# Kernel tuning notes

Measured on AMD Instinct MI355X. Metric: run time of the kernel, lower is better.

Reference implementation:

```python
import jax, jax.numpy as jnp
import numpy as np

# B images, N objects/image, R relations/image; D=obj/rel feature dim, H=GGNN hidden,
# NO=num object classes, NR=num relation classes, T=GGNN time steps.
B, N, R, D, H, NO, NR, T = 8, 64, 2048, 4096, 512, 151, 51, 3


def setup_inputs() -> dict:
    key = jax.random.key(0)
    ks = jax.random.split(key, 24)
    nrm = lambda k, shp: jax.random.normal(k, shp, dtype=jnp.float32) * 0.02
    im_inds = jnp.repeat(jnp.arange(B, dtype=jnp.int32), N)          # sorted per-object image ids
    img_r = jnp.repeat(jnp.arange(B, dtype=jnp.int32), R)            # per-relation image ids
    pair = jax.random.randint(ks[0], (B * R, 2), 0, N, dtype=jnp.int32) + (img_r * N)[:, None]
    rel_inds = jnp.concatenate([img_r[:, None], pair], axis=1)        # [B*R, 3]
    return dict(
        im_inds=im_inds, rel_inds=rel_inds,
        obj_fmaps=jax.random.normal(ks[1], (B * N, D), jnp.float32),
        obj_logits=jax.random.normal(ks[2], (B * N, NO), jnp.float32),
        vr=jax.random.normal(ks[3], (B * R, D), jnp.float32),
        W_obj=nrm(ks[4], (D, H)), b_obj=jnp.zeros((H,), jnp.float32),
        W_rel=nrm(ks[5], (D, H)), b_rel=jnp.zeros((H,), jnp.float32),
        W_prob=nrm(ks[6], (NO, H)), b_prob=jnp.zeros((H,), jnp.float32),
        W_so=nrm(ks[7], (H, H)), W_oo=nrm(ks[8], (H, H)),
        W_rs=nrm(ks[9], (H, H)), W_ro=nrm(ks[10], (H, H)),
        Wz=nrm(ks[11], (H, H)), Uz=nrm(ks[12], (H, H)), bz=jnp.zeros((H,), jnp.float32),
        Wr=nrm(ks[13], (H, H)), Ur=nrm(ks[14], (H, H)), br=jnp.zeros((H,), jnp.float32),
        Wh=nrm(ks[15], (H, H)), Uh=nrm(ks[16], (H, H)), bh=jnp.zeros((H,), jnp.float32),
        W_out_rel=nrm(ks[17], (2 * H, H)), b_out_rel=jnp.zeros((H,), jnp.float32),
        W_cls_rel=nrm(ks[18], (H, NR)), b_cls_rel=jnp.zeros((NR,), jnp.float32),
        W_out_obj=nrm(ks[19], (2 * H, H)), b_out_obj=jnp.zeros((H,), jnp.float32),
        W_cls_obj=nrm(ks[20], (H, NO)), b_cls_obj=jnp.zeros((NO,), jnp.float32),
    )


def reference(im_inds, rel_inds, obj_fmaps, obj_logits, vr,
              W_obj, b_obj, W_rel, b_rel, W_prob, b_prob,
              W_so, W_oo, W_rs, W_ro,
              Wz, Uz, bz, Wr, Ur, br, Wh, Uh, bh,
              W_out_rel, b_out_rel, W_cls_rel, b_cls_rel,
              W_out_obj, b_out_obj, W_cls_obj, b_cls_obj):
    # obj_probs = softmax(obj_logits); project features + class distribution into GGNN hidden
    obj_probs = jax.nn.softmax(obj_logits, axis=-1)
    xo = (obj_fmaps @ W_obj + b_obj + obj_probs @ W_prob + b_prob).reshape(B, N, H)
    xr = (vr @ W_rel + b_rel).reshape(B, R, H)
    # per-image local indices: rel_inds[rel_s:rel_e, 1:] - obj_s
    off = (jnp.arange(B, dtype=rel_inds.dtype) * N)[:, None]
    subj = rel_inds[:, 1].reshape(B, R) - off
    objn = rel_inds[:, 2].reshape(B, R) - off

    def gru(h, m):
        z = jax.nn.sigmoid(m @ Wz + h @ Uz + bz)
        r = jax.nn.sigmoid(m @ Wr + h @ Ur + br)
        hh = jnp.tanh(m @ Wh + (r * h) @ Uh + bh)
        return (1.0 - z) * h + z * hh

    def per_image(xo_i, xr_i, s, o):
        ho, hr = xo_i, xr_i
        for _ in range(T):  # fixed recurrence depth (time_step_num)
            mr = ho[s] @ W_so + ho[o] @ W_oo                               # gather obj -> rel
            mo = (jax.ops.segment_sum(hr @ W_rs, s, num_segments=N)
                  + jax.ops.segment_sum(hr @ W_ro, o, num_segments=N))     # scatter rel -> obj
            ho, hr = gru(ho, mo), gru(hr, mr)
        rel_logits = jnp.tanh(jnp.concatenate([hr, xr_i], -1) @ W_out_rel + b_out_rel) @ W_cls_rel + b_cls_rel
        obj_ref = jnp.tanh(jnp.concatenate([ho, xo_i], -1) @ W_out_obj + b_out_obj) @ W_cls_obj + b_cls_obj
        return rel_logits, obj_ref

    rel_logits, obj_ref = jax.vmap(per_image)(xo, xr, subj, objn)
    rel_logits = rel_logits.reshape(B * R, NR)
    obj_ref = obj_ref.reshape(B * N, NO)
    scpred_softmax = jax.nn.softmax(rel_logits, axis=-1)
    scent_softmax = jax.nn.softmax(obj_ref, axis=-1)
    # sgcls, inference, no obj_labels: obj_preds = argmax over classes 1..NO-1, + 1
    obj_preds = jnp.argmax(obj_ref[:, 1:], axis=-1) + 1
    return (obj_ref, obj_preds, rel_logits, scpred_softmax, scent_softmax)
```

## Files before the change

### kernel.cpp

```cpp
#include <hip/hip_runtime.h>
#include <math.h>

#define Bn   8
#define Nn   64
#define Rn   2048
#define Dn   4096
#define Hn   512
#define NOc  151
#define NRc  51
#define Tt   3
#define BNt  (Bn*Nn)
#define BRt  (Bn*Rn)
#define Mall (BRt+BNt)

typedef __attribute__((ext_vector_type(8))) short short8;
typedef __attribute__((ext_vector_type(4))) float f32x4;

__device__ __forceinline__ float sigmf(float x){ return 1.0f/(1.0f+expf(-x)); }

__device__ __forceinline__ ushort f2bf_rne(float x){
  unsigned u = __float_as_uint(x);
  unsigned r = u + 0x7FFFu + ((u>>16)&1u);
  return (ushort)(r>>16);
}
__device__ __forceinline__ float bf2f(ushort h){
  return __uint_as_float(((unsigned)h)<<16);
}

__device__ __forceinline__ void async_ld16(const ushort* g, ushort* l){
  __builtin_amdgcn_global_load_lds(
      (const __attribute__((address_space(1))) unsigned int*)g,
      (__attribute__((address_space(3))) unsigned int*)l, 16, 0, 0);
}

template<int BM,int BN,int ASPLIT>
__global__ __launch_bounds__(256)
void gemm_b3(const float* __restrict__ Af,
             const ushort* __restrict__ Aph, const ushort* __restrict__ Apl,
             const ushort* __restrict__ Bhg, const ushort* __restrict__ Blg,
             float* __restrict__ Cf, const float* __restrict__ Cin,
             int M,int N,int K,int lda,int ldb,int ldc,
             const float* __restrict__ bias, const float* __restrict__ bias2,
             int act,int dupoff,
             ushort* __restrict__ Cph, ushort* __restrict__ Cpl,int ldcp,int dupp,
             int swz,int mode,const int* __restrict__ rel,
             const float* __restrict__ Gso,const float* __restrict__ G1,
             int brt,float* __restrict__ Zb,
             ushort* __restrict__ RHh,ushort* __restrict__ RHl,
             float* __restrict__ Hf,
             ushort* __restrict__ HXph,ushort* __restrict__ HXpl)
{
  constexpr int MT = BM/32, NT = BN/32;
  constexpr int NSEG = BN/16;
  constexpr int SEGW = NSEG/2;
  __shared__ ushort As[2][2][BM*32];
  __shared__ ushort Bs[2][2][BN*32];

  int bxi = blockIdx.x, byi = blockIdx.y;
  if (swz){
    int id  = byi*gridDim.x + bxi;
    int mch = gridDim.y >> 3;
    int xcd = id & 7, j = id >> 3;
    byi = xcd*mch + j % mch;
    bxi = j / mch;
  }
  const int tid  = threadIdx.x;
  const int lane = tid & 63;
  const int wid  = tid >> 6;
  const int quad = lane >> 4, l15 = lane & 15;
  const int wm = (wid>>1)*(BM/2), wn = (wid&1)*(BN/2);
  const int bm = byi*BM, bn = bxi*BN;

  constexpr int TPR = 256/BM, CPT = 32/TPR;
  const int ar = tid / TPR;
  const int ak = (tid % TPR) * CPT;
  const int grA = bm + ar;
  const int aswz = (ar>>1)&3;

  const ushort* bptr[SEGW];
#pragma unroll
  for (int i=0;i<SEGW;i++){
    int seg = i*4 + wid;
    int plane = (seg >= NSEG) ? 1 : 0;
    int ss = seg & (NSEG-1);
    int row = ss*16 + (lane>>2);
    int cg = (lane&3) ^ ((row>>1)&3);
    bptr[i] = (plane ? Blg : Bhg) + (size_t)(bn + row)*ldb + cg*8;
  }

  f32x4 acc[MT][NT];
#pragma unroll
  for (int i=0;i<MT;i++)
#pragma unroll
    for (int j=0;j<NT;j++) acc[i][j] = (f32x4){0.f,0.f,0.f,0.f};

  float  avf[ASPLIT ? 1 : CPT];
  short8 avh[ASPLIT ? CPT/8 : 1], avl[ASPLIT ? CPT/8 : 1];

  auto load_A = [&](int k0){
    if constexpr (ASPLIT){
      if (grA < M){
#pragma unroll
        for (int i=0;i<CPT/8;i++){
          avh[i] = *(const short8*)(Aph + (size_t)grA*lda + k0 + ak + i*8);
          avl[i] = *(const short8*)(Apl + (size_t)grA*lda + k0 + ak + i*8);
        }
      } else {
#pragma unroll
        for (int i=0;i<CPT/8;i++){
#pragma unroll
          for (int q=0;q<8;q++){ avh[i][q]=0; avl[i][q]=0; }
        }
      }
    } else {
      if (grA < M && ((lda&3)==0) && k0 + ak + CPT <= K) {
        const float* p = Af + (size_t)grA*lda + k0 + ak;
#pragma unroll
        for (int i=0;i<CPT/4;i++) ((float4*)avf)[i] = ((const float4*)p)[i];
      } else {
#pragma unroll
        for (int i=0;i<CPT;i++){
          int gk = k0+ak+i;
          avf[i] = (grA<M && gk<K) ? Af[(size_t)grA*lda+gk] : 0.f;
        }
      }
    }
  };

  auto issue_B = [&](int k0,int buf){
#pragma unroll
    for (int i=0;i<SEGW;i++){
      int seg = i*4 + wid;
      int plane = (seg >= NSEG) ? 1 : 0;
      int ss = seg & (NSEG-1);
      async_ld16(bptr[i] + k0, &Bs[buf][plane][ss*512]);
    }
  };

  auto stage_A = [&](int buf){
    if constexpr (ASPLIT){
#pragma unroll
      for (int i=0;i<CPT/8;i++){
        int pos = (ak/8 + i) ^ aswz;
        *(short8*)&As[buf][0][ar*32 + pos*8] = avh[i];
        *(short8*)&As[buf][1][ar*32 + pos*8] = avl[i];
      }
    } else {
      ushort hs[CPT], ls[CPT];
#pragma unroll
      for (int i=0;i<CPT;i++){
        ushort h = f2bf_rne(avf[i]);
        hs[i]=h; ls[i]=f2bf_rne(avf[i]-bf2f(h));
      }
#pragma unroll
      for (int i=0;i<CPT;i+=8){
        short8 vh, vl;
#pragma unroll
        for (int q=0;q<8;q++){ vh[q]=(short)hs[i+q]; vl[q]=(short)ls[i+q]; }
        int pos = ((ak+i)/8) ^ aswz;
        *(short8*)&As[buf][0][ar*32 + pos*8] = vh;
        *(short8*)&As[buf][1][ar*32 + pos*8] = vl;
      }
    }
  };

  auto compute = [&](int buf){
    short8 afh[MT], afl[MT], bfh[NT], bfl[NT];
#pragma unroll
    for (int i=0;i<MT;i++){
      int row = wm + i*16 + l15;
      int o = row*32 + ((quad ^ ((row>>1)&3))*8);
      afh[i] = *(const short8*)&As[buf][0][o];
      afl[i] = *(const short8*)&As[buf][1][o];
    }
#pragma unroll
    for (int j=0;j<NT;j++){
      int row = wn + j*16 + l15;
      int o = row*32 + ((quad ^ ((row>>1)&3))*8);
      bfh[j] = *(const short8*)&Bs[buf][0][o];
      bfl[j] = *(const short8*)&Bs[buf][1][o];
    }
#pragma unroll
    for (int i=0;i<MT;i++)
#pragma unroll
      for (int j=0;j<NT;j++)
        acc[i][j] = __builtin_amdgcn_mfma_f32_16x16x32_bf16(afh[i], bfh[j], acc[i][j], 0,0,0);
#pragma unroll
    for (int i=0;i<MT;i++)
#pragma unroll
      for (int j=0;j<NT;j++)
        acc[i][j] = __builtin_amdgcn_mfma_f32_16x16x32_bf16(afh[i], bfl[j], acc[i][j], 0,0,0);
#pragma unroll
    for (int i=0;i<MT;i++)
#pragma unroll
      for (int j=0;j<NT;j++)
        acc[i][j] = __builtin_amdgcn_mfma_f32_16x16x32_bf16(afl[i], bfh[j], acc[i][j], 0,0,0);
  };

  load_A(0);
  issue_B(0, 0);
  stage_A(0);
  __syncthreads();

  int cur = 0;
  for (int k0 = 0; k0 < K; k0 += 32){
    if (k0 + 32 < K){
      load_A(k0+32);
      issue_B(k0+32, cur^1);
      compute(cur);
      stage_A(cur^1);
    } else {
      compute(cur);
    }
    __syncthreads();
    cur ^= 1;
  }

  if (mode == 0) {
#pragma unroll
    for (int i=0;i<MT;i++){
      int gm0 = bm + wm + i*16 + quad*4;
#pragma unroll
      for (int j=0;j<NT;j++){
        int gn = bn + wn + j*16 + l15;
        if (gn >= N) continue;
#pragma unroll
        for (int r=0;r<4;r++){
          int gm = gm0 + r;
          if (gm >= M) continue;
          float v = acc[i][j][r];
          if (Cin)  v += Cin[(size_t)gm*ldc+gn];
          if (bias) v += bias[gn];
          if (act==1) v = sigmf(v);
          else if (act==2) v = tanhf(v);
          if (Cf){
            Cf[(size_t)gm*ldc+gn] = v;
            if (dupoff) Cf[(size_t)gm*ldc+gn+dupoff] = v;
          }
          if (Cph){
            ushort h_ = f2bf_rne(v);
            ushort l_ = f2bf_rne(v - bf2f(h_));
            size_t p = (size_t)gm*ldcp + gn;
            Cph[p]=h_; Cpl[p]=l_;
            if (dupp){ Cph[p+dupp]=h_; Cpl[p+dupp]=l_; }
          }
        }
      }
    }
  } else if (mode == 1) {
#pragma unroll
    for (int i=0;i<MT;i++){
#pragma unroll
      for (int r=0;r<4;r++){
        int gm = bm + wm + i*16 + quad*4 + r;
        if (gm >= M) continue;
        bool isrel = gm < brt;
        int s=0,o=0; const float* g1row = nullptr;
        if (isrel){ s = rel[gm*3+1]; o = rel[gm*3+2]; }
        else g1row = G1 + (size_t)(gm-brt)*1536;
#pragma unroll
        for (int j=0;j<NT;j++){
          int gn = bn + wn + j*16 + l15;
          float v = acc[i][j][r];
          if (gn < 512){
            float g = isrel ? Gso[(size_t)s*3072+gn] + Gso[(size_t)o*3072+1536+gn]
                            : g1row[gn];
            Zb[(size_t)gm*512+gn] = sigmf(v + g + bias[gn]);
          } else {
            int h = gn - 512;
            float g = isrel ? Gso[(size_t)s*3072+512+h] + Gso[(size_t)o*3072+2048+h]
                            : g1row[512+h];
            float rhv = sigmf(v + g + bias2[h]) * Hf[(size_t)gm*512+h];
            ushort h_ = f2bf_rne(rhv);
            ushort l_ = f2bf_rne(rhv - bf2f(h_));
            RHh[(size_t)gm*512+h]=h_; RHl[(size_t)gm*512+h]=l_;
          }
        }
      }
    }
  } else {
#pragma unroll
    for (int i=0;i<MT;i++){
#pragma unroll
      for (int r=0;r<4;r++){
        int gm = bm + wm + i*16 + quad*4 + r;
        if (gm >= M) continue;
        bool isrel = gm < brt;
        int s=0,o=0; const float* g1row = nullptr;
        if (isrel){ s = rel[gm*3+1]; o = rel[gm*3+2]; }
        else g1row = G1 + (size_t)(gm-brt)*1536;
#pragma unroll
        for (int j=0;j<NT;j++){
          int h = bn + wn + j*16 + l15;
          float v = acc[i][j][r];
          float g = isrel ? Gso[(size_t)s*3072+1024+h] + Gso[(size_t)o*3072+2560+h]
                          : g1row[1024+h];
          float hh = tanhf(v + g + bias[h]);
          size_t ix = (size_t)gm*512+h;
          float z = Zb[ix];
          float hn = (1.f-z)*Hf[ix] + z*hh;
          Hf[ix] = hn;
          ushort h_ = f2bf_rne(hn);
          ushort l_ = f2bf_rne(hn - bf2f(h_));
          size_t p = (size_t)gm*1024+h;
          HXph[p]=h_; HXpl[p]=l_;
        }
      }
    }
  }
}

__global__ __launch_bounds__(256)
void tsplit(const float* __restrict__ src,int K,int N,
            ushort* __restrict__ dh, ushort* __restrict__ dl,
            int dld,int rowoff,int koff,int Npad)
{
  __shared__ float t[32][33];
  const int tx = threadIdx.x, ty = threadIdx.y;
  const int kb = blockIdx.x*32, nb = blockIdx.y*32;
#pragma unroll
  for (int r=0;r<4;r++){
    int k = kb + ty + r*8, n = nb + tx;
    t[ty+r*8][tx] = (k<K && n<N) ? src[(size_t)k*N + n] : 0.f;
  }
  __syncthreads();
#pragma unroll
  for (int r=0;r<4;r++){
    int n = nb + ty + r*8, k = kb + tx;
    if (n < Npad){
      float v = t[tx][ty+r*8];
      ushort h = f2bf_rne(v);
      ushort l = f2bf_rne(v - bf2f(h));
      size_t o = (size_t)(rowoff+n)*dld + koff + k;
      dh[o]=h; dl[o]=l;
    }
  }
}

__global__ __launch_bounds__(64)
void softmax_kernel(const float* __restrict__ in, float* __restrict__ out,
                    int cols, int ldi, int ldo, int padto)
{
  int row = blockIdx.x, lane = threadIdx.x;
  const float* rp = in + (size_t)row*ldi;
  float m = -INFINITY;
  for (int c = lane; c < cols; c += 64) m = fmaxf(m, rp[c]);
  for (int off = 32; off; off >>= 1) m = fmaxf(m, __shfl_xor(m, off));
  float s = 0.f;
  for (int c = lane; c < cols; c += 64) s += expf(rp[c]-m);
  for (int off = 32; off; off >>= 1) s += __shfl_xor(s, off);
  float inv = 1.f/s;
  float* op = out + (size_t)row*ldo;
  for (int c = lane; c < padto; c += 64)
    op[c] = (c < cols) ? expf(rp[c]-m)*inv : 0.f;
}

__global__ __launch_bounds__(64)
void argmax_kernel(const float* __restrict__ ref, float* __restrict__ preds)
{
  int row = blockIdx.x, lane = threadIdx.x;
  const float* rp = ref + (size_t)row*NOc;
  float bv = -INFINITY; int bi = NOc;
  for (int c = 1+lane; c < NOc; c += 64) { float v = rp[c]; if (v > bv) { bv=v; bi=c; } }
  for (int off=32; off; off>>=1) {
    float ov = __shfl_xor(bv, off); int oi = __shfl_xor(bi, off);
    if (ov > bv || (ov == bv && oi < bi)) { bv = ov; bi = oi; }
  }
  if (lane==0) preds[row] = (float)bi;
}

__global__ __launch_bounds__(64)
void segsum2(const float* __restrict__ Hf, const int* __restrict__ rel_inds,
             float* __restrict__ SumSO)
{
  __shared__ float accS[64][64];
  __shared__ float accO[64][64];
  const int t = threadIdx.x;
  const int hb = blockIdx.x*64;
  const int img = blockIdx.z;
  const int relbase = img*Rn + blockIdx.y*(Rn/4);
  for (int ob=0; ob<64; ob++){ accS[ob][t]=0.f; accO[ob][t]=0.f; }
  for (int i=0;i<Rn/4;i++){
    int r = relbase+i;
    int s = rel_inds[r*3+1] - img*64;
    int o = rel_inds[r*3+2] - img*64;
    float v = Hf[(size_t)r*512 + hb + t];
    accS[s][t]+=v; accO[o][t]+=v;
  }
  for (int ob=0;ob<64;ob++){
    size_t rowb = (size_t)(img*64+ob)*1024 + hb + t;
    atomicAdd(&SumSO[rowb],     accS[ob][t]);
    atomicAdd(&SumSO[rowb+512], accO[ob][t]);
  }
}

#define FZ0 0,nullptr,nullptr,nullptr,0,nullptr,nullptr,nullptr,nullptr,nullptr,nullptr

static void TS(hipStream_t s,const float*src,int K,int N,ushort*dh,ushort*dl,
               int dld,int rowoff,int koff,int Kpad,int Npad){
  dim3 g(Kpad/32,(Npad+31)/32);
  tsplit<<<g,dim3(32,8),0,s>>>(src,K,N,dh,dl,dld,rowoff,koff,Npad);
}

extern "C" void kernel_launch(void* const* d_in, const int* in_sizes, int n_in,
                              void* d_out, int out_size, void* d_ws, size_t ws_size,
                              hipStream_t stream) {
  (void)in_sizes; (void)n_in; (void)out_size; (void)ws_size;
  const int*   rel_inds   = (const int*)  d_in[1];
  const float* obj_fmaps  = (const float*)d_in[2];
  const float* obj_logits = (const float*)d_in[3];
  const float* vr         = (const float*)d_in[4];
  const float* W_obj      = (const float*)d_in[5];
  const float* b_obj      = (const float*)d_in[6];
  const float* W_rel      = (const float*)d_in[7];
  const float* b_rel      = (const float*)d_in[8];
  const float* W_prob     = (const float*)d_in[9];
  const float* b_prob     = (const float*)d_in[10];
  const float* W_so       = (const float*)d_in[11];
  const float* W_oo       = (const float*)d_in[12];
  const float* W_rs       = (const float*)d_in[13];
  const float* W_ro       = (const float*)d_in[14];
  const float* Wz         = (const float*)d_in[15];
  const float* Uz         = (const float*)d_in[16];
  const float* bz         = (const float*)d_in[17];
  const float* Wr         = (const float*)d_in[18];
  const float* Ur         = (const float*)d_in[19];
  const float* br         = (const float*)d_in[20];
  const float* Wh         = (const float*)d_in[21];
  const float* Uh         = (const float*)d_in[22];
  const float* bh         = (const float*)d_in[23];
  const float* W_out_rel  = (const float*)d_in[24];
  const float* b_out_rel  = (const float*)d_in[25];
  const float* W_cls_rel  = (const float*)d_in[26];
  const float* b_cls_rel  = (const float*)d_in[27];
  const float* W_out_obj  = (const float*)d_in[28];
  const float* b_out_obj  = (const float*)d_in[29];
  const float* W_cls_obj  = (const float*)d_in[30];
  const float* b_cls_obj  = (const float*)d_in[31];

  float* out          = (float*)d_out;
  float* out_obj_ref  = out;
  float* out_preds    = out + 77312;
  float* out_rel_log  = out + 77824;
  float* out_scpred   = out + 913408;
  float* out_scent    = out + 1748992;

  char* base = (char*)d_ws; size_t off = 0;
  auto alloc = [&](size_t bytes)->void*{ void* p = base+off; off = (off+bytes+255)&~(size_t)255; return p; };
  float*  Hf    = (float*) alloc((size_t)Mall*512*4);
  ushort* HXph  = (ushort*)alloc((size_t)Mall*1024*2);
  ushort* HXpl  = (ushort*)alloc((size_t)Mall*1024*2);
  ushort* RHh   = (ushort*)alloc((size_t)Mall*512*2);
  ushort* RHl   = (ushort*)alloc((size_t)Mall*512*2);
  float*  Zb    = (float*) alloc((size_t)Mall*512*4);
  ushort* Bt3h  = (ushort*)alloc((size_t)1536*512*2);
  ushort* Bt3l  = (ushort*)alloc((size_t)1536*512*2);
  ushort* BtU2h = (ushort*)alloc((size_t)1024*512*2);
  ushort* BtU2l = (ushort*)alloc((size_t)1024*512*2);
  ushort* BtUHh = (ushort*)alloc((size_t)512*512*2);
  ushort* BtUHl = (ushort*)alloc((size_t)512*512*2);
  ushort* BtPh  = (ushort*)alloc((size_t)1536*1024*2);
  ushort* BtPl  = (ushort*)alloc((size_t)1536*1024*2);
  ushort* BtORh = (ushort*)alloc((size_t)512*1024*2);
  ushort* BtORl = (ushort*)alloc((size_t)512*1024*2);
  ushort* BtCRh = (ushort*)alloc((size_t)64*512*2);
  ushort* BtCRl = (ushort*)alloc((size_t)64*512*2);
  ushort* BtOOh = (ushort*)alloc((size_t)512*1024*2);
  ushort* BtOOl = (ushort*)alloc((size_t)512*1024*2);
  ushort* BtCOh = (ushort*)alloc((size_t)192*512*2);
  ushort* BtCOl = (ushort*)alloc((size_t)192*512*2);
  ushort* BtWCh = (ushort*)alloc((size_t)3072*512*2);
  ushort* BtWCl = (ushort*)alloc((size_t)3072*512*2);
  float*  Gso   = (float*) alloc((size_t)512*3072*4);
  float*  G1    = (float*) alloc((size_t)512*1536*4);
  float*  SumSO = (float*) alloc((size_t)512*1024*4);
  float*  oprob = (float*) alloc((size_t)512*152*4);
  float*  Xotmp = (float*) alloc((size_t)512*512*4);
  ushort* COph  = (ushort*)alloc((size_t)512*512*2);
  ushort* COpl  = (ushort*)alloc((size_t)512*512*2);

  ushort* BtRELh = (ushort*)Zb;
  ushort* BtRELl = BtRELh + (size_t)512*4096;
  ushort* BtOBJh = BtRELl + (size_t)512*4096;
  ushort* BtOBJl = BtOBJh + (size_t)512*4096;
  ushort* BtPRh  = BtOBJl + (size_t)512*4096;
  ushort* BtPRl  = BtPRh  + (size_t)512*160;
  float*  Wcat   = (float*)(BtPRl + (size_t)512*160);
  float*  Pfp    = Wcat + (size_t)512*3072;

  softmax_kernel<<<512,64,0,stream>>>(obj_logits, oprob, NOc, NOc, 152, 152);
  TS(stream, W_rel,  4096,512, BtRELh,BtRELl, 4096, 0,0, 4096, 512);
  TS(stream, W_obj,  4096,512, BtOBJh,BtOBJl, 4096, 0,0, 4096, 512);
  TS(stream, W_prob,  151,512, BtPRh, BtPRl,   160, 0,0,  160, 512);
  TS(stream, Wz, 512,512, Bt3h,Bt3l, 512,    0,0, 512, 512);
  TS(stream, Wr, 512,512, Bt3h,Bt3l, 512,  512,0, 512, 512);
  TS(stream, Wh, 512,512, Bt3h,Bt3l, 512, 1024,0, 512, 512);
  TS(stream, Uz, 512,512, BtU2h,BtU2l, 512,   0,0, 512, 512);
  TS(stream, Ur, 512,512, BtU2h,BtU2l, 512, 512,0, 512, 512);
  TS(stream, Uh, 512,512, BtUHh,BtUHl, 512, 0,0, 512, 512);
  TS(stream, W_out_rel, 1024,512, BtORh,BtORl, 1024, 0,0, 1024, 512);
  TS(stream, W_cls_rel,  512, 51, BtCRh,BtCRl,  512, 0,0,  512, 64);
  TS(stream, W_out_obj, 1024,512, BtOOh,BtOOl, 1024, 0,0, 1024, 512);
  TS(stream, W_cls_obj,  512,151, BtCOh,BtCOl,  512, 0,0,  512, 192);

  {
    dim3 g(8,8);
    gemm_b3<64,64,0><<<g,256,0,stream>>>(obj_fmaps,nullptr,nullptr,BtOBJh,BtOBJl,
      Xotmp,nullptr, 512,512,4096, 4096,4096,512, b_obj,nullptr,0,0,
      nullptr,nullptr,0,0, 1, FZ0);
    gemm_b3<64,64,0><<<g,256,0,stream>>>(oprob,nullptr,nullptr,BtPRh,BtPRl,
      Hf+(size_t)BRt*512, Xotmp, 512,512,151, 152,160,512, b_prob,nullptr,0,0,
      HXph+(size_t)BRt*1024+512, HXpl+(size_t)BRt*1024+512, 1024, -512, 1, FZ0);
  }
  {
    dim3 g(2,256);
    gemm_b3<64,256,0><<<g,256,0,stream>>>(vr,nullptr,nullptr,BtRELh,BtRELl,
      Hf,nullptr, BRt,512,4096, 4096,4096,512, b_rel,nullptr,0,0,
      HXph+512, HXpl+512, 1024, -512, 1, FZ0);
  }
  {
    dim3 g(24,8);
    gemm_b3<64,64,0><<<g,256,0,stream>>>(W_so,nullptr,nullptr,Bt3h,Bt3l,
      Wcat,nullptr, 512,1536,512, 512,512,3072, nullptr,nullptr,0,0, nullptr,nullptr,0,0, 1, FZ0);
    gemm_b3<64,64,0><<<g,256,0,stream>>>(W_oo,nullptr,nullptr,Bt3h,Bt3l,
      Wcat+1536,nullptr, 512,1536,512, 512,512,3072, nullptr,nullptr,0,0, nullptr,nullptr,0,0, 1, FZ0);
    gemm_b3<64,64,0><<<g,256,0,stream>>>(W_rs,nullptr,nullptr,Bt3h,Bt3l,
      Pfp,nullptr, 512,1536,512, 512,512,1536, nullptr,nullptr,0,0, nullptr,nullptr,0,0, 1, FZ0);
    gemm_b3<64,64,0><<<g,256,0,stream>>>(W_ro,nullptr,nullptr,Bt3h,Bt3l,
      Pfp+(size_t)512*1536,nullptr, 512,1536,512, 512,512,1536, nullptr,nullptr,0,0, nullptr,nullptr,0,0, 1, FZ0);
  }
  TS(stream, Wcat,  512,3072, BtWCh,BtWCl,  512, 0,0,  512, 3072);
  TS(stream, Pfp,  1024,1536, BtPh, BtPl,  1024, 0,0, 1024, 1536);

  for (int t = 0; t < Tt; t++) {
    {
      dim3 g(48,8);
      gemm_b3<64,64,1><<<g,256,0,stream>>>(nullptr,HXph+(size_t)BRt*1024,HXpl+(size_t)BRt*1024,
        BtWCh,BtWCl, Gso,nullptr, 512,3072,512, 1024,512,3072,
        nullptr,nullptr,0,0, nullptr,nullptr,0,0, 1, FZ0);
    }
    hipMemsetAsync(SumSO, 0, (size_t)512*1024*4, stream);
    segsum2<<<dim3(8,4,8),64,0,stream>>>(Hf, rel_inds, SumSO);
    {
      dim3 g(24,8);
      gemm_b3<64,64,0><<<g,256,0,stream>>>(SumSO,nullptr,nullptr,BtPh,BtPl,
        G1,nullptr, 512,1536,1024, 1024,1024,1536,
        nullptr,nullptr,0,0, nullptr,nullptr,0,0, 1, FZ0);
    }
    {
      dim3 g(8,136);
      gemm_b3<128,128,1><<<g,256,0,stream>>>(nullptr,HXph,HXpl,BtU2h,BtU2l,
        nullptr,nullptr, Mall,1024,512, 1024,512,0, bz,br,0,0,
        nullptr,nullptr,0,0, 1,
        1, rel_inds, Gso, G1, BRt, Zb, RHh,RHl, Hf, nullptr,nullptr);
    }
    {
      dim3 g(4,136);
      gemm_b3<128,128,1><<<g,256,0,stream>>>(nullptr,RHh,RHl,BtUHh,BtUHl,
        nullptr,nullptr, Mall,512,512, 512,512,0, bh,nullptr,0,0,
        nullptr,nullptr,0,0, 1,
        2, rel_inds, Gso, G1, BRt, Zb, nullptr,nullptr, Hf, HXph,HXpl);
    }
  }

  {
    dim3 g(4,128);
    gemm_b3<128,128,1><<<g,256,0,stream>>>(nullptr,HXph,HXpl,BtORh,BtORl,
      nullptr,nullptr, BRt,512,1024, 1024,1024,0, b_out_rel,nullptr,2,0,
      RHh,RHl,512,0, 1, FZ0);
  }
  {
    dim3 g(1,256);
    gemm_b3<64,64,1><<<g,256,0,stream>>>(nullptr,RHh,RHl,BtCRh,BtCRl,
      out_rel_log,nullptr, BRt,NRc,512, 512,512,NRc, b_cls_rel,nullptr,0,0,
      nullptr,nullptr,0,0, 1, FZ0);
  }
  softmax_kernel<<<BRt,64,0,stream>>>(out_rel_log, out_scpred, NRc, NRc, NRc, NRc);
  {
    dim3 g(8,8);
    gemm_b3<64,64,1><<<g,256,0,stream>>>(nullptr,HXph+(size_t)BRt*1024,HXpl+(size_t)BRt*1024,
      BtOOh,BtOOl, nullptr,nullptr, 512,512,1024, 1024,1024,0, b_out_obj,nullptr,2,0,
      COph,COpl,512,0, 1, FZ0);
  }
  {
    dim3 g(3,8);
    gemm_b3<64,64,1><<<g,256,0,stream>>>(nullptr,COph,COpl,BtCOh,BtCOl,
      out_obj_ref,nullptr, 512,NOc,512, 512,512,NOc, b_cls_obj,nullptr,0,0,
      nullptr,nullptr,0,0, 1, FZ0);
  }
  softmax_kernel<<<512,64,0,stream>>>(out_obj_ref, out_scent, NOc, NOc, NOc, NOc);
  argmax_kernel<<<512,64,0,stream>>>(out_obj_ref, out_preds);
}
```

Baseline: 2.494 ms.

## Double-buffer A register prefetch two tiles ahead with explicit vmcnt waits

```diff
diff --git a/kernel.cpp b/kernel.cpp
--- a/kernel.cpp
+++ b/kernel.cpp
@@ -32,6 +32,9 @@
       (const __attribute__((address_space(1))) unsigned int*)g,
       (__attribute__((address_space(3))) unsigned int*)l, 16, 0, 0);
 }
+
+#define WAITB(N) asm volatile("s_waitcnt vmcnt(" #N ") lgkmcnt(0)" ::: "memory")
+#define SB0 __builtin_amdgcn_sched_barrier(0)
 
 template<int BM,int BN,int ASPLIT>
 __global__ __launch_bounds__(256)
@@ -72,6 +75,7 @@
   const int bm = byi*BM, bn = bxi*BN;
 
   constexpr int TPR = 256/BM, CPT = 32/TPR;
+  constexpr int AOUT = CPT/4;
   const int ar = tid / TPR;
   const int ak = (tid % TPR) * CPT;
   const int grA = bm + ar;
@@ -94,34 +98,38 @@
 #pragma unroll
     for (int j=0;j<NT;j++) acc[i][j] = (f32x4){0.f,0.f,0.f,0.f};
 
-  float  avf[ASPLIT ? 1 : CPT];
-  short8 avh[ASPLIT ? CPT/8 : 1], avl[ASPLIT ? CPT/8 : 1];
-
-  auto load_A = [&](int k0){
+  struct ARegs {
+    float  f[ASPLIT ? 1 : CPT];
+    short8 h[ASPLIT ? CPT/8 : 1];
+    short8 l[ASPLIT ? CPT/8 : 1];
+  };
+  ARegs a0, a1;
+
+  auto load_A = [&](ARegs& a, int k0){
     if constexpr (ASPLIT){
       if (grA < M){
 #pragma unroll
         for (int i=0;i<CPT/8;i++){
-          avh[i] = *(const short8*)(Aph + (size_t)grA*lda + k0 + ak + i*8);
-          avl[i] = *(const short8*)(Apl + (size_t)grA*lda + k0 + ak + i*8);
+          a.h[i] = *(const short8*)(Aph + (size_t)grA*lda + k0 + ak + i*8);
+          a.l[i] = *(const short8*)(Apl + (size_t)grA*lda + k0 + ak + i*8);
         }
       } else {
 #pragma unroll
         for (int i=0;i<CPT/8;i++){
 #pragma unroll
-          for (int q=0;q<8;q++){ avh[i][q]=0; avl[i][q]=0; }
+          for (int q=0;q<8;q++){ a.h[i][q]=0; a.l[i][q]=0; }
         }
       }
     } else {
-      if (grA < M && ((lda&3)==0) && k0 + ak + CPT <= K) {
+      if (grA < M && ((lda&3)==0) && k0 + 32 <= K) {
         const float* p = Af + (size_t)grA*lda + k0 + ak;
 #pragma unroll
-        for (int i=0;i<CPT/4;i++) ((float4*)avf)[i] = ((const float4*)p)[i];
+        for (int i=0;i<CPT/4;i++) ((float4*)a.f)[i] = ((const float4*)p)[i];
       } else {
 #pragma unroll
         for (int i=0;i<CPT;i++){
           int gk = k0+ak+i;
-          avf[i] = (grA<M && gk<K) ? Af[(size_t)grA*lda+gk] : 0.f;
+          a.f[i] = (grA<M && gk<K) ? Af[(size_t)grA*lda+gk] : 0.f;
         }
       }
     }
@@ -137,20 +145,20 @@
     }
   };
 
-  auto stage_A = [&](int buf){
+  auto stage_A = [&](ARegs& a, int buf){
     if constexpr (ASPLIT){
 #pragma unroll
       for (int i=0;i<CPT/8;i++){
         int pos = (ak/8 + i) ^ aswz;
-        *(short8*)&As[buf][0][ar*32 + pos*8] = avh[i];
-        *(short8*)&As[buf][1][ar*32 + pos*8] = avl[i];
+        *(short8*)&As[buf][0][ar*32 + pos*8] = a.h[i];
+        *(short8*)&As[buf][1][ar*32 + pos*8] = a.l[i];
       }
     } else {
       ushort hs[CPT], ls[CPT];
 #pragma unroll
       for (int i=0;i<CPT;i++){
-        ushort h = f2bf_rne(avf[i]);
-        hs[i]=h; ls[i]=f2bf_rne(avf[i]-bf2f(h));
+        ushort h = f2bf_rne(a.f[i]);
+        hs[i]=h; ls[i]=f2bf_rne(a.f[i]-bf2f(h));
       }
 #pragma unroll
       for (int i=0;i<CPT;i+=8){
@@ -197,23 +205,53 @@
         acc[i][j] = __builtin_amdgcn_mfma_f32_16x16x32_bf16(afl[i], bfh[j], acc[i][j], 0,0,0);
   };
 
-  load_A(0);
+  load_A(a0, 0);
   issue_B(0, 0);
-  stage_A(0);
-  __syncthreads();
-
-  int cur = 0;
-  for (int k0 = 0; k0 < K; k0 += 32){
-    if (k0 + 32 < K){
-      load_A(k0+32);
-      issue_B(k0+32, cur^1);
+  SB0;
+  if (32 < K) load_A(a1, 32);
+  stage_A(a0, 0);
+  if (32 < K) { if constexpr (AOUT==4) WAITB(4); else WAITB(2); }
+  else WAITB(0);
+  SB0;
+  __builtin_amdgcn_s_barrier();
+  SB0;
+
+  int k0 = 0, cur = 0;
+  while (true) {
+    {
+      bool h1 = k0+32 < K, h2 = k0+64 < K;
+      if (h1) issue_B(k0+32, cur^1);
+      SB0;
+      if (h2) load_A(a0, k0+64);
       compute(cur);
-      stage_A(cur^1);
-    } else {
+      if (h1) {
+        stage_A(a1, cur^1);
+        if (h2) { if constexpr (AOUT==4) WAITB(4); else WAITB(2); }
+        else WAITB(0);
+        SB0;
+        __builtin_amdgcn_s_barrier();
+        SB0;
+      }
+      k0 += 32; cur ^= 1;
+      if (!h1) break;
+    }
+    {
+      bool h1 = k0+32 < K, h2 = k0+64 < K;
+      if (h1) issue_B(k0+32, cur^1);
+      SB0;
+      if (h2) load_A(a1, k0+64);
       compute(cur);
-    }
-    __syncthreads();
-    cur ^= 1;
+      if (h1) {
+        stage_A(a0, cur^1);
+        if (h2) { if constexpr (AOUT==4) WAITB(4); else WAITB(2); }
+        else WAITB(0);
+        SB0;
+        __builtin_amdgcn_s_barrier();
+        SB0;
+      }
+      k0 += 32; cur ^= 1;
+      if (!h1) break;
+    }
   }
 
   if (mode == 0) {
```

Result: no change. 2.460 ms (-1.4%).
